# Kernel optimization log

Measured on AMD Instinct MI355X. Metric: run time of the kernel, lower is better.

The kernel has to match this reference:

```python
import jax, jax.numpy as jnp
import numpy as np

PAD = 2
STRIDE = 1

def _cayley(sig):
    # Geometric-product Cayley table G[i, j, k]: e_i * e_j = G[i, j, i^j] e_{i^j}
    # Blades indexed by bitmask over generators; sig = metric signature (+1/-1 per generator).
    n = len(sig)
    dim = 1 << n
    G = np.zeros((dim, dim, dim), dtype=np.float32)
    for a in range(dim):
        for b in range(dim):
            s = 0
            aa = a >> 1
            while aa:
                s += bin(aa & b).count('1')
                aa >>= 1
            sign = -1.0 if (s & 1) else 1.0
            common = a & b
            for i, m in enumerate(sig):
                if (common >> i) & 1:
                    sign *= m
            G[a, b, a ^ b] = sign
    return G


def setup_inputs() -> dict:
    key = jax.random.key(0)
    k1, k2, k3 = jax.random.split(key, 3)
    B, C, O, BD, L, K = 8, 64, 64, 8, 4096, 5
    x = jax.random.normal(k1, (B, C, BD, L), dtype=jnp.float32)
    bound = 1.0 / np.sqrt(C * BD * K)  # kaiming-style uniform bound
    W = jax.random.uniform(k2, (K, C, O, BD), minval=-bound, maxval=bound, dtype=jnp.float32)
    b = jax.random.uniform(k3, (1, O, BD, 1), minval=-bound, maxval=bound, dtype=jnp.float32)
    G = jnp.asarray(_cayley((1.0, 1.0, 1.0)))  # Cl(3,0), basis_dim = 8
    return {"x": x, "W": W, "b": b, "G": G}


def reference(x, W, b, G):
    # Original: pad length dim, unfold windows, then
    # result[b,o,k,w] = sum_{i,j,c,v} G[i,j,k] * W[v,c,o,i] * x_pad[b,c,j,w+v], plus bias.
    # Equivalent efficient form: pre-contract G with W into a conv kernel over
    # fused (channel, basis) axes and run a standard 1D convolution.
    K = W.shape[0]
    B, C, J, L = x.shape
    O = W.shape[2]
    Kb = G.shape[2]
    xp = jnp.pad(x, ((0, 0), (0, 0), (0, 0), (PAD, PAD)))  # padding_mode='zeros'
    # T[o,k,c,j,v] = sum_i G[i,j,k] W[v,c,o,i]  (tiny tensor: O*Kb x C*J x K)
    kern = jnp.einsum('ijk,vcoi->okcjv', G, W).reshape(O * Kb, C * J, K)
    xin = xp.reshape(B, C * J, L + 2 * PAD)
    out = jax.lax.conv_general_dilated(
        xin, kern, window_strides=(STRIDE,), padding='VALID',
        dimension_numbers=('NCH', 'OIH', 'NCH'))
    # out channels are (o major, k minor) per the reshape above
    return out.reshape(B, O, Kb, out.shape[-1]) + b
```

## Files before the change

### kernel.cpp

```cpp
#include <hip/hip_runtime.h>


#define C_    64
#define L_    4096
#define PAD_  2
#define OKch  512
#define XSTR  4104

#define BM    128
#define BN    128
#define BKCJ  64
#define NCJB  8
#define NV    5
#define TILE  8192
#define WIN   132
#define BSZ   (WIN * 64)

typedef __bf16 bf16x8 __attribute__((ext_vector_type(8)));
typedef float floatx4 __attribute__((ext_vector_type(4)));

__device__ __forceinline__ unsigned short f2bf(float f) {
    unsigned int u = __float_as_uint(f);
    u += 0x7FFFu + ((u >> 16) & 1u);
    return (unsigned short)(u >> 16);
}

#define WAIT_LGKM_0() asm volatile("s_waitcnt lgkmcnt(0)" ::: "memory")
#define WAITV_(N) asm volatile("s_waitcnt vmcnt(" #N ")" ::: "memory")
#define WAITV(N) do { WAITV_(N); __builtin_amdgcn_sched_barrier(0); } while (0)

__device__ __forceinline__ void barrier_raw() {
    asm volatile("" ::: "memory");
    __builtin_amdgcn_sched_barrier(0);
    __builtin_amdgcn_s_barrier();
    __builtin_amdgcn_sched_barrier(0);
    asm volatile("" ::: "memory");
}

#define GLD_U32(dst, ptr) \
    asm volatile("global_load_dword %0, %1, off" : "=&v"(dst) : "v"(ptr))
#define GLD_A4(a0, a1, a2, a3, ptr)                          \
    asm volatile("global_load_dwordx4 %0, %4, off\n\t"       \
                 "global_load_dwordx4 %1, %4, off offset:1024\n\t" \
                 "global_load_dwordx4 %2, %4, off offset:2048\n\t" \
                 "global_load_dwordx4 %3, %4, off offset:3072"     \
                 : "=&v"(a0), "=&v"(a1), "=&v"(a2), "=&v"(a3) : "v"(ptr))

__global__ __launch_bounds__(256) void prep(
    const float* __restrict__ W, const float* __restrict__ G,
    const float* __restrict__ x,
    unsigned short* __restrict__ kernT, unsigned short* __restrict__ xp)
{
    const int bid = blockIdx.x;
    const int tid = threadIdx.x;
    if (bid < 640) {
        __shared__ float Gs[512];
        Gs[tid] = G[tid];
        Gs[tid + 256] = G[tid + 256];
        __syncthreads();

        const int idx  = bid * 256 + tid;
        const int lrow = idx & 15;
        const int quad = (idx >> 4) & 3;
        const int f    = (idx >> 6) & 15;
        const int mq   = f >> 1;
        const int kk2  = f & 1;
        const int t    = idx >> 10;
        const int v    = t % 5;
        const int tc   = t / 5;
        const int cjb  = tc & 7;
        const int y    = tc >> 3;
        const int m    = (mq << 4) | lrow;
        const int ok   = (y << 7) | m;
        const int o    = ok >> 3;
        const int kb   = ok & 7;
        const int c    = (cjb << 3) | (kk2 << 2) | quad;

        const float* Wp = W + (((v * C_ + c) * 64 + o) << 3);
        const float4 w0 = *(const float4*)Wp;
        const float4 w1 = *(const float4*)(Wp + 4);
        const float w[8] = {w0.x, w0.y, w0.z, w0.w, w1.x, w1.y, w1.z, w1.w};

        unsigned int pk[4];
        #pragma unroll
        for (int j = 0; j < 8; j++) {
            float s = 0.f;
            #pragma unroll
            for (int i = 0; i < 8; i++)
                s += Gs[i * 64 + j * 8 + kb] * w[i];
            const unsigned short h = f2bf(s);
            if (j & 1) pk[j >> 1] |= (unsigned int)h << 16;
            else       pk[j >> 1]  = h;
        }
        uint4 uu; uu.x = pk[0]; uu.y = pk[1]; uu.z = pk[2]; uu.w = pk[3];
        *reinterpret_cast<uint4*>(
            &kernT[((size_t)t << 13) + (f << 9) + (quad << 7) + (lrow << 3)]) = uu;
    } else {
        const int row = bid - 640;
        const float* src = x + (size_t)row * L_;
        unsigned short* dst = xp + (size_t)row * XSTR;
        #pragma unroll
        for (int i = 0; i < 4; i++) {
            const int p = (i * 256 + tid) << 2;
            const float4 fv = *reinterpret_cast<const float4*>(src + p);
            const unsigned int u0 = (unsigned int)f2bf(fv.x) | ((unsigned int)f2bf(fv.y) << 16);
            const unsigned int u1 = (unsigned int)f2bf(fv.z) | ((unsigned int)f2bf(fv.w) << 16);
            *reinterpret_cast<unsigned int*>(dst + 2 + p) = u0;
            *reinterpret_cast<unsigned int*>(dst + 4 + p) = u1;
        }
        if (tid == 0) {
            *reinterpret_cast<unsigned int*>(dst) = 0u;
            *reinterpret_cast<unsigned int*>(dst + 4098) = 0u;
        }
    }
}

__device__ __forceinline__ void bi_round(const unsigned short* xp, int cj0,
                                         int w0, int round, unsigned int (&d)[8]) {
    const int idx  = round * 256 + (int)threadIdx.x;
    const int kgrp = idx / 66;
    const int wp   = idx - kgrp * 66;
    const unsigned short* p =
        xp + (size_t)(cj0 + (kgrp << 3)) * XSTR + (size_t)(w0 + (wp << 1));
    GLD_U32(d[0], p);
    GLD_U32(d[1], p + XSTR);
    GLD_U32(d[2], p + 2 * XSTR);
    GLD_U32(d[3], p + 3 * XSTR);
    GLD_U32(d[4], p + 4 * XSTR);
    GLD_U32(d[5], p + 5 * XSTR);
    GLD_U32(d[6], p + 6 * XSTR);
    GLD_U32(d[7], p + 7 * XSTR);
}

__device__ __forceinline__ void bi_tail(const unsigned short* xp, int cj0,
                                        int w0, unsigned int (&d)[8]) {
    const int lane = (int)threadIdx.x & 63;
    const int wave = (int)threadIdx.x >> 6;
    if ((lane & 15) == 0) {
        const int idx  = 512 + (wave << 2) + (lane >> 4);
        const int kgrp = idx / 66;
        const int wp   = idx - kgrp * 66;
        const unsigned short* p =
            xp + (size_t)(cj0 + (kgrp << 3)) * XSTR + (size_t)(w0 + (wp << 1));
        GLD_U32(d[0], p);
        GLD_U32(d[1], p + XSTR);
        GLD_U32(d[2], p + 2 * XSTR);
        GLD_U32(d[3], p + 3 * XSTR);
        GLD_U32(d[4], p + 4 * XSTR);
        GLD_U32(d[5], p + 5 * XSTR);
        GLD_U32(d[6], p + 6 * XSTR);
        GLD_U32(d[7], p + 7 * XSTR);
    }
}

__device__ __forceinline__ void st_item(unsigned short* Bw, int kgrp, int nn,
                                        const unsigned int (&d)[8]) {
    const unsigned int lo0 = (d[0] & 0xffffu) | (d[1] << 16);
    const unsigned int hi0 = (d[0] >> 16)     | (d[1] & 0xffff0000u);
    const unsigned int lo1 = (d[2] & 0xffffu) | (d[3] << 16);
    const unsigned int hi1 = (d[2] >> 16)     | (d[3] & 0xffff0000u);
    const unsigned int lo2 = (d[4] & 0xffffu) | (d[5] << 16);
    const unsigned int hi2 = (d[4] >> 16)     | (d[5] & 0xffff0000u);
    const unsigned int lo3 = (d[6] & 0xffffu) | (d[7] << 16);
    const unsigned int hi3 = (d[6] >> 16)     | (d[7] & 0xffff0000u);
    const int s = kgrp ^ (nn & 7);
    uint4 Lv; Lv.x = lo0; Lv.y = lo1; Lv.z = lo2; Lv.w = lo3;
    uint4 Hv; Hv.x = hi0; Hv.y = hi1; Hv.z = hi2; Hv.w = hi3;
    *reinterpret_cast<uint4*>(&Bw[(nn << 6) + (s << 3)]) = Lv;
    *reinterpret_cast<uint4*>(&Bw[((nn + 1) << 6) + ((s ^ 1) << 3)]) = Hv;
}

__device__ __forceinline__ void st_round(unsigned short* Bw, int round,
                                         const unsigned int (&d)[8]) {
    const int idx  = round * 256 + (int)threadIdx.x;
    const int kgrp = idx / 66;
    const int wp   = idx - kgrp * 66;
    st_item(Bw, kgrp, wp << 1, d);
}

__device__ __forceinline__ void st_tail(unsigned short* Bw,
                                        const unsigned int (&d)[8]) {
    const int lane = (int)threadIdx.x & 63;
    const int wave = (int)threadIdx.x >> 6;
    if ((lane & 15) == 0) {
        const int idx  = 512 + (wave << 2) + (lane >> 4);
        const int kgrp = idx / 66;
        const int wp   = idx - kgrp * 66;
        st_item(Bw, kgrp, wp << 1, d);
    }
}

__device__ __forceinline__ void bfread(const unsigned short* BsR, int v, int kk2,
                                       int lrow, int quad, bf16x8 (&f)[8]) {
    const int s7  = (lrow + v) & 7;
    const int col = ((((kk2) << 2) | quad) ^ s7) << 3;
    const int rb  = (lrow + v) << 6;
    #pragma unroll
    for (int nt = 0; nt < 8; nt++)
        f[nt] = *reinterpret_cast<const bf16x8*>(&BsR[rb + (nt << 10) + col]);
}

__device__ __forceinline__ void cl(const bf16x8 (&a)[4], int kk2,
                                   const bf16x8 (&f)[8], floatx4 (&acc)[2][8]) {
    __builtin_amdgcn_s_setprio(1);
    #pragma unroll
    for (int mt = 0; mt < 2; mt++)
        #pragma unroll
        for (int nt = 0; nt < 8; nt++)
            acc[mt][nt] = __builtin_amdgcn_mfma_f32_16x16x32_bf16(
                a[mt * 2 + kk2], f[nt], acc[mt][nt], 0, 0, 0);
    __builtin_amdgcn_s_setprio(0);
}

__global__ __launch_bounds__(256, 2) void gpconv_mfma(
    const unsigned short* __restrict__ xp, const unsigned short* __restrict__ kernT,
    const float* __restrict__ bias, float* __restrict__ out)
{
    __shared__ unsigned short Bs[2 * BSZ];

    const int tid  = threadIdx.x;
    const int lane = tid & 63;
    const int wave = tid >> 6;
    const int lrow = lane & 15;
    const int quad = lane >> 4;

    const int bid = blockIdx.x;
    const int y   = (bid >> 3) & 3;
    const int xw  = ((bid >> 5) << 3) + (bid & 7);
    const int b   = xw >> 5;
    const int w0  = (xw & 31) * BN;
    const int mBase = y * BM;
    const unsigned short* xb = xp + (size_t)b * (size_t)(512 * XSTR);
    const unsigned short* ky = kernT + (size_t)(y * NCJB) * NV * TILE;
    const unsigned short* abase = ky + (wave << 11) + (lane << 3);

    floatx4 acc[2][8];
    {
        const floatx4 z = {0.f, 0.f, 0.f, 0.f};
        #pragma unroll
        for (int i2 = 0; i2 < 2; i2++)
            #pragma unroll
            for (int j2 = 0; j2 < 8; j2++) acc[i2][j2] = z;
    }

    bf16x8 aX[4], aY[4];
    unsigned int dA[8], dB[8], dT[8];

    bi_round(xb, 0, w0, 0, dA);
    bi_round(xb, 0, w0, 1, dB);
    bi_tail(xb, 0, w0, dT);
    GLD_A4(aX[0], aX[1], aX[2], aX[3], abase);
    WAITV(4);
    st_round(Bs, 0, dA);
    st_round(Bs, 1, dB);
    st_tail(Bs, dT);
    WAIT_LGKM_0();
    barrier_raw();

#define PHASE(CUR, NXT, CJB, V, STG, LASTP, WCMP)                             \
    {                                                                         \
        const unsigned short* BsR = Bs + (((CJB) & 1) ? BSZ : 0);             \
        unsigned short*       BsW = Bs + (((CJB) & 1) ? 0 : BSZ);             \
        if ((STG) && (V) == 3) { WAITV(4); st_round(BsW, 0, dA); }            \
        if ((STG) && (V) == 4) { WAITV(4); st_round(BsW, 1, dB);              \
                                 st_tail(BsW, dT); }                          \
        bf16x8 f0[8], f1[8];                                                  \
        bfread(BsR, (V), 0, lrow, quad, f0);                                  \
        if ((STG) && (V) == 2) bi_round(xb, ((CJB) + 1) * BKCJ, w0, 0, dA);   \
        if ((STG) && (V) == 3) { bi_round(xb, ((CJB) + 1) * BKCJ, w0, 1, dB); \
                                 bi_tail(xb, ((CJB) + 1) * BKCJ, w0, dT); }   \
        if (!(LASTP)) GLD_A4(NXT[0], NXT[1], NXT[2], NXT[3],                  \
                             abase + (size_t)((CJB) * 5 + (V) + 1) * TILE);   \
        WAITV(WCMP);                                                          \
        cl(CUR, 0, f0, acc);                                                  \
        bfread(BsR, (V), 1, lrow, quad, f1);                                  \
        cl(CUR, 1, f1, acc);                                                  \
        if ((STG) && (V) == 4) { WAIT_LGKM_0(); barrier_raw(); }              \
    }

    for (int cp = 0; cp < 3; cp++) {
        const int c0 = cp * 2, c1 = c0 + 1;
        PHASE(aX, aY, c0, 0, 1, 0, 4);
        PHASE(aY, aX, c0, 1, 1, 0, 4);
        PHASE(aX, aY, c0, 2, 1, 0, 12);
        PHASE(aY, aX, c0, 3, 1, 0, 20);
        PHASE(aX, aY, c0, 4, 1, 0, 4);
        PHASE(aY, aX, c1, 0, 1, 0, 4);
        PHASE(aX, aY, c1, 1, 1, 0, 4);
        PHASE(aY, aX, c1, 2, 1, 0, 12);
        PHASE(aX, aY, c1, 3, 1, 0, 20);
        PHASE(aY, aX, c1, 4, 1, 0, 4);
    }
    PHASE(aX, aY, 6, 0, 1, 0, 4);
    PHASE(aY, aX, 6, 1, 1, 0, 4);
    PHASE(aX, aY, 6, 2, 1, 0, 12);
    PHASE(aY, aX, 6, 3, 1, 0, 20);
    PHASE(aX, aY, 6, 4, 1, 0, 4);
    PHASE(aY, aX, 7, 0, 0, 0, 4);
    PHASE(aX, aY, 7, 1, 0, 0, 4);
    PHASE(aY, aX, 7, 2, 0, 0, 4);
    PHASE(aX, aY, 7, 3, 0, 0, 4);
    PHASE(aY, aX, 7, 4, 0, 1, 0);
#undef PHASE

    #pragma unroll
    for (int mt = 0; mt < 2; mt++) {
        #pragma unroll
        for (int e = 0; e < 4; e++) {
            const int okc = mBase + (wave << 5) + (mt << 4) + (quad << 2) + e;
            const float bv = bias[okc];
            float* orow = out + ((size_t)b * OKch + (size_t)okc) * L_ + w0;
            #pragma unroll
            for (int nt = 0; nt < 8; nt++) {
                const int n = (nt << 4) + lrow;
                orow[n] = acc[mt][nt][e] + bv;
            }
        }
    }
}

extern "C" void kernel_launch(void* const* d_in, const int* in_sizes, int n_in,
                              void* d_out, int out_size, void* d_ws, size_t ws_size,
                              hipStream_t stream) {
    const float* x    = (const float*)d_in[0];
    const float* W    = (const float*)d_in[1];
    const float* bias = (const float*)d_in[2];
    const float* G    = (const float*)d_in[3];
    unsigned short* kernT = (unsigned short*)d_ws;
    unsigned short* xp    = (unsigned short*)((char*)d_ws + (4 << 20));
    float* out = (float*)d_out;

    prep<<<dim3(640 + 4096), 256, 0, stream>>>(W, G, x, kernT, xp);
    gpconv_mfma<<<dim3(1024), 256, 0, stream>>>(xp, kernT, bias, out);
}
```

Measured before the change: 178.3 us.

## Switch wave tiling from 32x128 strips to 2x2 grid of 64x64 tiles

Re-partitions the 128x128 block tile among the four waves as a 2x2 grid of 64x64 sub-tiles instead of four 32x128 row strips. Each wave now loads twice as many A fragments from global (8 dwordx4 per phase) but reads half as many B fragments from LDS, which rebalances LDS read traffic against global/VGPR traffic. The vmcnt wait thresholds are adjusted to the larger number of loads in flight. The A prefetch registers double, which raises VGPR pressure under launch_bounds(256,2).

```diff
diff --git a/kernel.cpp b/kernel.cpp
--- a/kernel.cpp
+++ b/kernel.cpp
@@ -39,12 +39,18 @@
 
 #define GLD_U32(dst, ptr) \
     asm volatile("global_load_dword %0, %1, off" : "=&v"(dst) : "v"(ptr))
-#define GLD_A4(a0, a1, a2, a3, ptr)                          \
-    asm volatile("global_load_dwordx4 %0, %4, off\n\t"       \
-                 "global_load_dwordx4 %1, %4, off offset:1024\n\t" \
-                 "global_load_dwordx4 %2, %4, off offset:2048\n\t" \
-                 "global_load_dwordx4 %3, %4, off offset:3072"     \
-                 : "=&v"(a0), "=&v"(a1), "=&v"(a2), "=&v"(a3) : "v"(ptr))
+#define GLD_A8(a0, a1, a2, a3, a4, a5, a6, a7, p0, p1)             \
+    asm volatile("global_load_dwordx4 %0, %8, off\n\t"             \
+                 "global_load_dwordx4 %1, %8, off offset:1024\n\t" \
+                 "global_load_dwordx4 %2, %8, off offset:2048\n\t" \
+                 "global_load_dwordx4 %3, %8, off offset:3072\n\t" \
+                 "global_load_dwordx4 %4, %9, off\n\t"             \
+                 "global_load_dwordx4 %5, %9, off offset:1024\n\t" \
+                 "global_load_dwordx4 %6, %9, off offset:2048\n\t" \
+                 "global_load_dwordx4 %7, %9, off offset:3072"     \
+                 : "=&v"(a0), "=&v"(a1), "=&v"(a2), "=&v"(a3),     \
+                   "=&v"(a4), "=&v"(a5), "=&v"(a6), "=&v"(a7)      \
+                 : "v"(p0), "v"(p1))
 
 __global__ __launch_bounds__(256) void prep(
     const float* __restrict__ W, const float* __restrict__ G,
@@ -190,23 +196,24 @@
     }
 }
 
-__device__ __forceinline__ void bfread(const unsigned short* BsR, int v, int kk2,
-                                       int lrow, int quad, bf16x8 (&f)[8]) {
+__device__ __forceinline__ void bfread(const unsigned short* BsR, int wn, int v,
+                                       int kk2, int lrow, int quad,
+                                       bf16x8 (&f)[4]) {
     const int s7  = (lrow + v) & 7;
     const int col = ((((kk2) << 2) | quad) ^ s7) << 3;
-    const int rb  = (lrow + v) << 6;
+    const int rb  = (wn + lrow + v) << 6;
     #pragma unroll
-    for (int nt = 0; nt < 8; nt++)
+    for (int nt = 0; nt < 4; nt++)
         f[nt] = *reinterpret_cast<const bf16x8*>(&BsR[rb + (nt << 10) + col]);
 }
 
-__device__ __forceinline__ void cl(const bf16x8 (&a)[4], int kk2,
-                                   const bf16x8 (&f)[8], floatx4 (&acc)[2][8]) {
+__device__ __forceinline__ void cl(const bf16x8 (&a)[8], int kk2,
+                                   const bf16x8 (&f)[4], floatx4 (&acc)[4][4]) {
     __builtin_amdgcn_s_setprio(1);
     #pragma unroll
-    for (int mt = 0; mt < 2; mt++)
-        #pragma unroll
-        for (int nt = 0; nt < 8; nt++)
+    for (int mt = 0; mt < 4; mt++)
+        #pragma unroll
+        for (int nt = 0; nt < 4; nt++)
             acc[mt][nt] = __builtin_amdgcn_mfma_f32_16x16x32_bf16(
                 a[mt * 2 + kk2], f[nt], acc[mt][nt], 0, 0, 0);
     __builtin_amdgcn_s_setprio(0);
@@ -223,6 +230,8 @@
     const int wave = tid >> 6;
     const int lrow = lane & 15;
     const int quad = lane >> 4;
+    const int wm   = (wave >> 1) << 6;
+    const int wn   = (wave & 1) << 6;
 
     const int bid = blockIdx.x;
     const int y   = (bid >> 3) & 3;
@@ -232,87 +241,92 @@
     const int mBase = y * BM;
     const unsigned short* xb = xp + (size_t)b * (size_t)(512 * XSTR);
     const unsigned short* ky = kernT + (size_t)(y * NCJB) * NV * TILE;
-    const unsigned short* abase = ky + (wave << 11) + (lane << 3);
-
-    floatx4 acc[2][8];
+    const unsigned short* abase = ky + ((wave >> 1) << 12) + (lane << 3);
+
+    floatx4 acc[4][4];
     {
         const floatx4 z = {0.f, 0.f, 0.f, 0.f};
         #pragma unroll
-        for (int i2 = 0; i2 < 2; i2++)
+        for (int i2 = 0; i2 < 4; i2++)
             #pragma unroll
-            for (int j2 = 0; j2 < 8; j2++) acc[i2][j2] = z;
-    }
-
-    bf16x8 aX[4], aY[4];
+            for (int j2 = 0; j2 < 4; j2++) acc[i2][j2] = z;
+    }
+
+    bf16x8 aX[8], aY[8];
     unsigned int dA[8], dB[8], dT[8];
 
     bi_round(xb, 0, w0, 0, dA);
     bi_round(xb, 0, w0, 1, dB);
     bi_tail(xb, 0, w0, dT);
-    GLD_A4(aX[0], aX[1], aX[2], aX[3], abase);
-    WAITV(4);
+    GLD_A8(aX[0], aX[1], aX[2], aX[3], aX[4], aX[5], aX[6], aX[7],
+           abase, abase + 2048);
+    WAITV(8);
     st_round(Bs, 0, dA);
     st_round(Bs, 1, dB);
     st_tail(Bs, dT);
     WAIT_LGKM_0();
     barrier_raw();
 
-#define PHASE(CUR, NXT, CJB, V, STG, LASTP, WCMP)                             \
+#define PHASE(CUR, NXT, CJB, V, STG, DO_PRE, WCMP)                            \
     {                                                                         \
         const unsigned short* BsR = Bs + (((CJB) & 1) ? BSZ : 0);             \
         unsigned short*       BsW = Bs + (((CJB) & 1) ? 0 : BSZ);             \
-        if ((STG) && (V) == 3) { WAITV(4); st_round(BsW, 0, dA); }            \
-        if ((STG) && (V) == 4) { WAITV(4); st_round(BsW, 1, dB);              \
+        if ((STG) && (V) == 3) { WAITV(8); st_round(BsW, 0, dA); }            \
+        if ((STG) && (V) == 4) { WAITV(8); st_round(BsW, 1, dB);              \
                                  st_tail(BsW, dT); }                          \
-        bf16x8 f0[8], f1[8];                                                  \
-        bfread(BsR, (V), 0, lrow, quad, f0);                                  \
+        bf16x8 f0[4], f1[4];                                                  \
+        bfread(BsR, wn, (V), 0, lrow, quad, f0);                              \
         if ((STG) && (V) == 2) bi_round(xb, ((CJB) + 1) * BKCJ, w0, 0, dA);   \
         if ((STG) && (V) == 3) { bi_round(xb, ((CJB) + 1) * BKCJ, w0, 1, dB); \
                                  bi_tail(xb, ((CJB) + 1) * BKCJ, w0, dT); }   \
-        if (!(LASTP)) GLD_A4(NXT[0], NXT[1], NXT[2], NXT[3],                  \
-                             abase + (size_t)((CJB) * 5 + (V) + 1) * TILE);   \
+        if (DO_PRE) {                                                         \
+            const unsigned short* ap =                                        \
+                abase + (size_t)((CJB) * 5 + (V) + 1) * TILE;                 \
+            GLD_A8(NXT[0], NXT[1], NXT[2], NXT[3],                            \
+                   NXT[4], NXT[5], NXT[6], NXT[7], ap, ap + 2048);            \
+        }                                                                     \
         WAITV(WCMP);                                                          \
         cl(CUR, 0, f0, acc);                                                  \
-        bfread(BsR, (V), 1, lrow, quad, f1);                                  \
+        bfread(BsR, wn, (V), 1, lrow, quad, f1);                              \
         cl(CUR, 1, f1, acc);                                                  \
         if ((STG) && (V) == 4) { WAIT_LGKM_0(); barrier_raw(); }              \
     }
 
     for (int cp = 0; cp < 3; cp++) {
         const int c0 = cp * 2, c1 = c0 + 1;
-        PHASE(aX, aY, c0, 0, 1, 0, 4);
-        PHASE(aY, aX, c0, 1, 1, 0, 4);
-        PHASE(aX, aY, c0, 2, 1, 0, 12);
-        PHASE(aY, aX, c0, 3, 1, 0, 20);
-        PHASE(aX, aY, c0, 4, 1, 0, 4);
-        PHASE(aY, aX, c1, 0, 1, 0, 4);
-        PHASE(aX, aY, c1, 1, 1, 0, 4);
-        PHASE(aY, aX, c1, 2, 1, 0, 12);
-        PHASE(aX, aY, c1, 3, 1, 0, 20);
-        PHASE(aY, aX, c1, 4, 1, 0, 4);
-    }
-    PHASE(aX, aY, 6, 0, 1, 0, 4);
-    PHASE(aY, aX, 6, 1, 1, 0, 4);
-    PHASE(aX, aY, 6, 2, 1, 0, 12);
-    PHASE(aY, aX, 6, 3, 1, 0, 20);
-    PHASE(aX, aY, 6, 4, 1, 0, 4);
-    PHASE(aY, aX, 7, 0, 0, 0, 4);
-    PHASE(aX, aY, 7, 1, 0, 0, 4);
-    PHASE(aY, aX, 7, 2, 0, 0, 4);
-    PHASE(aX, aY, 7, 3, 0, 0, 4);
-    PHASE(aY, aX, 7, 4, 0, 1, 0);
+        PHASE(aX, aY, c0, 0, 1, 1, 8);
+        PHASE(aY, aX, c0, 1, 1, 1, 8);
+        PHASE(aX, aY, c0, 2, 1, 1, 16);
+        PHASE(aY, aX, c0, 3, 1, 1, 24);
+        PHASE(aX, aY, c0, 4, 1, 1, 8);
+        PHASE(aY, aX, c1, 0, 1, 1, 8);
+        PHASE(aX, aY, c1, 1, 1, 1, 8);
+        PHASE(aY, aX, c1, 2, 1, 1, 16);
+        PHASE(aX, aY, c1, 3, 1, 1, 24);
+        PHASE(aY, aX, c1, 4, 1, 1, 8);
+    }
+    PHASE(aX, aY, 6, 0, 1, 1, 8);
+    PHASE(aY, aX, 6, 1, 1, 1, 8);
+    PHASE(aX, aY, 6, 2, 1, 1, 16);
+    PHASE(aY, aX, 6, 3, 1, 1, 24);
+    PHASE(aX, aY, 6, 4, 1, 1, 8);
+    PHASE(aY, aX, 7, 0, 0, 1, 8);
+    PHASE(aX, aY, 7, 1, 0, 1, 8);
+    PHASE(aY, aX, 7, 2, 0, 1, 8);
+    PHASE(aX, aY, 7, 3, 0, 1, 8);
+    PHASE(aY, aX, 7, 4, 0, 0, 0);
 #undef PHASE
 
     #pragma unroll
-    for (int mt = 0; mt < 2; mt++) {
+    for (int mt = 0; mt < 4; mt++) {
         #pragma unroll
         for (int e = 0; e < 4; e++) {
-            const int okc = mBase + (wave << 5) + (mt << 4) + (quad << 2) + e;
+            const int okc = mBase + wm + (mt << 4) + (quad << 2) + e;
             const float bv = bias[okc];
             float* orow = out + ((size_t)b * OKch + (size_t)okc) * L_ + w0;
             #pragma unroll
-            for (int nt = 0; nt < 8; nt++) {
-                const int n = (nt << 4) + lrow;
+            for (int nt = 0; nt < 4; nt++) {
+                const int n = wn + (nt << 4) + lrow;
                 orow[n] = acc[mt][nt][e] + bv;
             }
         }
```

Measured after the change: 180.8 us. Within noise of the previous version (+1.4%).
